# Kernel tuning notes

Measured on AMD Instinct MI355X. Metric: run time of the kernel, lower is better.

The kernel has to match this reference:

```python
import jax, jax.numpy as jnp
import numpy as np

IMG_H, IMG_W = 900, 1600
NUM_CLASSES = 10
NUM_CAMS = 6

# pcdet boxes_to_corners_3d corner template (unit box, centered)
CORNER_TEMPLATE = jnp.array(
    [[1, 1, -1], [1, -1, -1], [-1, -1, -1], [-1, 1, -1],
     [1, 1, 1], [1, -1, 1], [-1, -1, 1], [-1, 1, 1]], dtype=jnp.float32) * 0.5


def boxes_to_corners_3d(boxes):
    # boxes: [N,7] = (x,y,z,dx,dy,dz,heading) -> [N,8,3]
    dims = boxes[:, 3:6]
    corners = dims[:, None, :] * CORNER_TEMPLATE  # [N,8,3]
    yaw = boxes[:, 6]
    c, s = jnp.cos(yaw), jnp.sin(yaw)
    z = jnp.zeros_like(c)
    o = jnp.ones_like(c)
    # rotate_points_along_z: points @ [[c,s,0],[-s,c,0],[0,0,1]]
    rot = jnp.stack([c, s, z, -s, c, z, z, z, o], axis=-1).reshape(-1, 3, 3)
    corners = jnp.einsum('nkj,njm->nkm', corners, rot)
    return corners + boxes[:, None, 0:3]


def box_iou(a, b):
    # a: [M,4], b: [K,4] xyxy -> [M,K]
    lt = jnp.maximum(a[:, None, :2], b[None, :, :2])
    rb = jnp.minimum(a[:, None, 2:], b[None, :, 2:])
    wh = jnp.clip(rb - lt, 0.0)
    inter = wh[..., 0] * wh[..., 1]
    area_a = (a[:, 2] - a[:, 0]) * (a[:, 3] - a[:, 1])
    area_b = (b[:, 2] - b[:, 0]) * (b[:, 3] - b[:, 1])
    union = area_a[:, None] + area_b[None, :] - inter
    return jnp.where(union > 0, inter / union, 0.0)


def _project_boxes(pred_boxes, img_aug_matrix, lidar_aug_matrix, lidar2image):
    # batch index 0 (B=1); returns proj [6,N,4] and valid [6,N]
    N = pred_boxes.shape[0]
    corners = boxes_to_corners_3d(pred_boxes).reshape(-1, 3)  # [N*8,3]
    la = lidar_aug_matrix[0]
    pts = corners - la[:3, 3]
    pts = jnp.linalg.inv(la[:3, :3]) @ pts.T  # [3, N*8]
    l2i = lidar2image[0]
    cc = l2i[:, :3, :3] @ pts + l2i[:, :3, 3][:, :, None]  # [6,3,N*8]
    zc = jnp.clip(cc[:, 2, :], 1e-5, 1e5)
    xy = cc[:, :2, :] / zc[:, None, :]
    cc = jnp.concatenate([xy, zc[:, None, :]], axis=1)
    ia = img_aug_matrix[0]
    cc = ia[:, :3, :3] @ cc + ia[:, :3, 3][:, :, None]
    pix = jnp.transpose(cc[:, :2, :], (0, 2, 1))  # [6, N*8, 2]
    # .long() truncation (non-differentiable in original)
    pix = jax.lax.stop_gradient(pix).astype(jnp.int32)
    px = jnp.clip(pix[..., 0], 0, IMG_W)
    py = jnp.clip(pix[..., 1], 0, IMG_H)
    pix = jnp.stack([px, py], -1).reshape(NUM_CAMS, N, 8, 2).astype(pred_boxes.dtype)
    xy1 = pix.min(axis=2)  # [6,N,2]
    xy2 = pix.max(axis=2)
    valid = jnp.all((xy2 - xy1) > 0, axis=-1)  # [6,N]
    proj = jnp.concatenate([xy1, xy2], axis=-1)  # [6,N,4]
    return proj, valid


def setup_inputs() -> dict:
    rng = np.random.default_rng(0)
    N, M = 4096, 6144
    xy = rng.uniform(-40, 40, (N, 2))
    zc = rng.uniform(-1, 1, (N, 1))
    dims = rng.uniform(1.0, 4.0, (N, 3))
    yaw = rng.uniform(0, 2 * np.pi, (N, 1))
    pred_boxes = np.concatenate([xy, zc, dims, yaw], axis=1).astype(np.float32)
    # 6 cameras: pinhole intrinsics + yaw-spaced extrinsics
    K = np.array([[1000., 0., 800.], [0., 1000., 450.], [0., 0., 1.]])
    l2i = np.zeros((1, NUM_CAMS, 4, 4), np.float32)
    for ci, ang in enumerate(np.linspace(0, 2 * np.pi, NUM_CAMS, endpoint=False)):
        fwd = np.array([np.cos(ang), np.sin(ang), 0.])
        right = np.array([np.sin(ang), -np.cos(ang), 0.])
        down = np.array([0., 0., -1.])
        R = np.stack([right, down, fwd], 0)
        l2i[0, ci, :3, :3] = K @ R
        l2i[0, ci, 3, 3] = 1.0
    img_aug_matrix = np.tile(np.eye(4, dtype=np.float32), (1, NUM_CAMS, 1, 1))
    lidar_aug_matrix = np.eye(4, dtype=np.float32)[None]
    cx = rng.uniform(0, IMG_W, M)
    cy = rng.uniform(0, IMG_H, M)
    w = rng.uniform(20, 300, M)
    h = rng.uniform(20, 300, M)
    det_boxes = np.stack([np.clip(cx - w / 2, 0, IMG_W), np.clip(cy - h / 2, 0, IMG_H),
                          np.clip(cx + w / 2, 0, IMG_W), np.clip(cy + h / 2, 0, IMG_H)], 1).astype(np.float32)
    det_labels = rng.integers(1, NUM_CLASSES + 1, M).astype(np.int32)
    det_scores = rng.uniform(0.05, 1.0, M).astype(np.float32)
    det_batch_idx = np.zeros(M, np.int32)
    det_cam_idx = (np.arange(M) % NUM_CAMS).astype(np.int32)
    return {
        'pred_boxes': jnp.asarray(pred_boxes),
        'img_aug_matrix': jnp.asarray(img_aug_matrix),
        'lidar_aug_matrix': jnp.asarray(lidar_aug_matrix),
        'lidar2image': jnp.asarray(l2i),
        'det_boxes': jnp.asarray(det_boxes),
        'det_labels': jnp.asarray(det_labels),
        'det_scores': jnp.asarray(det_scores),
        'det_batch_idx': jnp.asarray(det_batch_idx),
        'det_cam_idx': jnp.asarray(det_cam_idx),
    }


def reference(pred_boxes, img_aug_matrix, lidar_aug_matrix, lidar2image,
              det_boxes, det_labels, det_scores, det_batch_idx, det_cam_idx):
    proj, valid = _project_boxes(pred_boxes, img_aug_matrix, lidar_aug_matrix, lidar2image)
    label_matrix = jax.nn.one_hot(det_labels - 1, NUM_CLASSES, dtype=det_scores.dtype) * det_scores[:, None]
    probs_sum = jnp.zeros((pred_boxes.shape[0], NUM_CLASSES), dtype=det_scores.dtype)
    for c in range(NUM_CAMS):
        mask = ((det_cam_idx == c) & (det_batch_idx == 0)).astype(det_boxes.dtype)
        iou = box_iou(det_boxes, proj[c]) * mask[:, None]  # [M,N]
        probs_sum = probs_sum + (iou.T @ label_matrix) * valid[c][:, None]  # [N,10]
    denom = 1e-5 + valid.astype(probs_sum.dtype).sum(axis=0)
    box_probs_mean = probs_sum / denom[:, None]
    pred_scores = jnp.nan_to_num(jnp.max(box_probs_mean, axis=-1), nan=0.0)
    pred_labels = jnp.argmax(box_probs_mean, axis=-1) + 1
    return pred_labels, pred_scores
```

## Files before the change

### kernel.cpp

```cpp
#include <hip/hip_runtime.h>
#include <cstdint>
#include <climits>

#pragma clang fp contract(off)

#define NCAM 6
#define NCLS 10
#define NKEY 60
#define IMGW 1600
#define IMGH 900
#define TBOX 4
#define CHUNK 512

__device__ __forceinline__ int sat_f2i(float f) {
    if (f != f) return 0;
    if (f >= 2147483648.0f) return INT_MAX;
    if (f <= -2147483648.0f) return INT_MIN;
    return (int)f;
}

__global__ __launch_bounds__(256) void prep_kernel(
        const float*  __restrict__ boxes,
        const float*  __restrict__ ia,
        const float*  __restrict__ la,
        const float*  __restrict__ l2i,
        const float4* __restrict__ det_boxes,
        const int*    __restrict__ det_labels,
        const float*  __restrict__ det_scores,
        const int*    __restrict__ det_batch,
        const int*    __restrict__ det_cam,
        float* __restrict__ projW,
        float* __restrict__ slab,
        int*   __restrict__ cnt,
        int N, int M, int PB, int CAPW) {
    int tid = threadIdx.x;

    if ((int)blockIdx.x < PB) {
        int n = blockIdx.x * 256 + tid;
        if (n >= N) return;
        float bx = boxes[n*7+0], by = boxes[n*7+1], bz = boxes[n*7+2];
        float dx = boxes[n*7+3], dy = boxes[n*7+4], dz = boxes[n*7+5];
        float yaw = boxes[n*7+6];
        float c = (float)cos((double)yaw);
        float s = (float)sin((double)yaw);

        float a00=la[0],a01=la[1],a02=la[2],t0=la[3];
        float a10=la[4],a11=la[5],a12=la[6],t1=la[7];
        float a20=la[8],a21=la[9],a22=la[10],t2=la[11];
        float det = a00*(a11*a22-a12*a21) - a01*(a10*a22-a12*a20) + a02*(a10*a21-a11*a20);
        float id = 1.0f/det;
        float r00=(a11*a22-a12*a21)*id, r01=(a02*a21-a01*a22)*id, r02=(a01*a12-a02*a11)*id;
        float r10=(a12*a20-a10*a22)*id, r11=(a00*a22-a02*a20)*id, r12=(a02*a10-a00*a12)*id;
        float r20=(a10*a21-a11*a20)*id, r21=(a01*a20-a00*a21)*id, r22=(a00*a11-a01*a10)*id;

        float PX[8], PY[8], PZ[8];
        #pragma unroll
        for (int k = 0; k < 8; k++) {
            float sx = ((k==0||k==1||k==4||k==5) ?  0.5f : -0.5f) * dx;
            float sy = ((k==0||k==3||k==4||k==7) ?  0.5f : -0.5f) * dy;
            float sz = ((k>=4)                   ?  0.5f : -0.5f) * dz;
            float cx = sx*c - sy*s + bx;
            float cy = sx*s + sy*c + by;
            float cz = sz + bz;
            float ux = cx - t0, uy = cy - t1, uz = cz - t2;
            PX[k] = r00*ux + r01*uy + r02*uz;
            PY[k] = r10*ux + r11*uy + r12*uz;
            PZ[k] = r20*ux + r21*uy + r22*uz;
        }
        for (int cam = 0; cam < NCAM; cam++) {
            const float* L = l2i + cam*16;
            const float* A = ia  + cam*16;
            int minx = INT_MAX, miny = INT_MAX, maxx = INT_MIN, maxy = INT_MIN;
            #pragma unroll
            for (int k = 0; k < 8; k++) {
                float u = L[0]*PX[k] + L[1]*PY[k] + L[2]*PZ[k]  + L[3];
                float v = L[4]*PX[k] + L[5]*PY[k] + L[6]*PZ[k]  + L[7];
                float w = L[8]*PX[k] + L[9]*PY[k] + L[10]*PZ[k] + L[11];
                float zc = fminf(fmaxf(w, 1e-5f), 100000.0f);
                float x = u / zc, y = v / zc;
                float xx = A[0]*x + A[1]*y + A[2]*zc + A[3];
                float yy = A[4]*x + A[5]*y + A[6]*zc + A[7];
                int pxi = sat_f2i(xx); pxi = min(max(pxi, 0), IMGW);
                int pyi = sat_f2i(yy); pyi = min(max(pyi, 0), IMGH);
                minx = min(minx, pxi); maxx = max(maxx, pxi);
                miny = min(miny, pyi); maxy = max(maxy, pyi);
            }
            float x1 = (float)minx, y1 = (float)miny, x2 = (float)maxx, y2 = (float)maxy;
            float validf = ((x2 - x1) > 0.0f && (y2 - y1) > 0.0f) ? 1.0f : 0.0f;
            projW[(cam*6+0)*N + n] = x1;
            projW[(cam*6+1)*N + n] = y1;
            projW[(cam*6+2)*N + n] = x2;
            projW[(cam*6+3)*N + n] = y2;
            projW[(cam*6+4)*N + n] = (x2 - x1) * (y2 - y1);
            projW[(cam*6+5)*N + n] = validf;
        }
        return;
    }

    int k = (int)blockIdx.x - PB;
    int cam = k / NCLS, cls = k % NCLS;
    int w = tid >> 6, lane = tid & 63;
    int per = (M + 3) >> 2;
    int m0 = w * per, m1 = min(m0 + per, M);
    float* base = slab + (size_t)(k * 4 + w) * CAPW * 8;
    int pos = 0;
    for (int c = m0; c < m1; c += 64) {
        int m = c + lane;
        bool pred = false;
        if (m < m1) {
            int dc = det_cam[m], db = det_batch[m], dl = det_labels[m] - 1;
            pred = (db == 0) && (dc == cam) && (dl == cls);
        }
        unsigned long long ball = __ballot(pred);
        if (pred) {
            int p = pos + __popcll(ball & ((1ull << lane) - 1ull));
            float4 b = det_boxes[m];
            float area = (b.z - b.x) * (b.w - b.y);
            float4* o = (float4*)(base + (size_t)p * 8);
            o[0] = b;
            o[1] = make_float4(area, det_scores[m], 0.0f, 0.0f);
        }
        pos += __popcll(ball);
    }
    if (lane == 0) cnt[k * 4 + w] = pos;
}

__global__ __launch_bounds__(256) void main_kernel(
        const float* __restrict__ projW,
        const float* __restrict__ slab,
        const int*   __restrict__ cnt,
        float*       __restrict__ partial,
        int N, int CAPW) {
    #pragma clang fp contract(fast)
    int tid = threadIdx.x;
    int k = blockIdx.y;
    int cam = k / NCLS;
    int box0 = blockIdx.x * (256 * TBOX) + tid;

    __shared__ float4 sbox[CHUNK];
    __shared__ float2 sq[CHUNK];

    float Px1[TBOX], Py1[TBOX], Px2[TBOX], Py2[TBOX], Pa[TBOX], Pv[TBOX], acc[TBOX];
    #pragma unroll
    for (int t = 0; t < TBOX; t++) {
        int b = box0 + t * 256;
        int bi = min(b, N - 1);
        Px1[t] = projW[(cam*6+0)*N + bi];
        Py1[t] = projW[(cam*6+1)*N + bi];
        Px2[t] = projW[(cam*6+2)*N + bi];
        Py2[t] = projW[(cam*6+3)*N + bi];
        Pa[t]  = projW[(cam*6+4)*N + bi];
        Pv[t]  = projW[(cam*6+5)*N + bi];
        acc[t] = 0.0f;
    }

    #pragma unroll
    for (int sub = 0; sub < 4; sub++) {
        int nk = cnt[k * 4 + sub];
        const float4* gb = (const float4*)(slab + (size_t)(k * 4 + sub) * CAPW * 8);
        for (int base = 0; base < nk; base += CHUNK) {
            int cc = min(CHUNK, nk - base);
            __syncthreads();
            for (int i = tid; i < cc; i += 256) {
                float4 b0 = gb[(size_t)(base + i) * 2];
                float4 b1 = gb[(size_t)(base + i) * 2 + 1];
                sbox[i] = b0;
                sq[i] = make_float2(b1.x, b1.y);
            }
            __syncthreads();
            for (int m = 0; m < cc; m++) {
                float4 b = sbox[m];
                float2 q = sq[m];
                #pragma unroll
                for (int t = 0; t < TBOX; t++) {
                    float ltx = fmaxf(b.x, Px1[t]);
                    float lty = fmaxf(b.y, Py1[t]);
                    float rbx = fminf(b.z, Px2[t]);
                    float rby = fminf(b.w, Py2[t]);
                    float iw = fmaxf(rbx - ltx, 0.0f);
                    float ih = fmaxf(rby - lty, 0.0f);
                    float inter = iw * ih;
                    float uni = (q.x + Pa[t]) - inter;
                    float r = __fdividef(inter, uni);
                    float iou = (uni > 0.0f) ? r : 0.0f;
                    acc[t] += iou * q.y;
                }
            }
        }
    }

    #pragma unroll
    for (int t = 0; t < TBOX; t++) {
        int b = box0 + t * 256;
        if (b < N) partial[(size_t)k * N + b] = acc[t] * Pv[t];
    }
}

__global__ __launch_bounds__(256) void reduce_kernel(
        const float* __restrict__ partial,
        const float* __restrict__ projW,
        float* __restrict__ out, int N) {
    int n = blockIdx.x * 256 + threadIdx.x;
    if (n >= N) return;
    float p[NCLS];
    #pragma unroll
    for (int c = 0; c < NCLS; c++) p[c] = 0.0f;
    #pragma unroll
    for (int cam = 0; cam < NCAM; cam++)
        #pragma unroll
        for (int c = 0; c < NCLS; c++)
            p[c] += partial[(size_t)(cam * NCLS + c) * N + n];
    float nv = 0.0f;
    #pragma unroll
    for (int cam = 0; cam < NCAM; cam++) nv += projW[(cam*6+5)*N + n];
    float denom = 1e-5f + nv;
    float best = -1e30f; int bk = 0;
    #pragma unroll
    for (int c = 0; c < NCLS; c++) {
        float v = p[c] / denom;
        if (v > best) { best = v; bk = c; }
    }
    out[n]     = (float)(bk + 1);
    out[N + n] = best;
}

extern "C" void kernel_launch(void* const* d_in, const int* in_sizes, int n_in,
                              void* d_out, int out_size, void* d_ws, size_t ws_size,
                              hipStream_t stream) {
    const float*  pred_boxes = (const float*)d_in[0];
    const float*  ia         = (const float*)d_in[1];
    const float*  la         = (const float*)d_in[2];
    const float*  l2i        = (const float*)d_in[3];
    const float4* det_boxes  = (const float4*)d_in[4];
    const int*    det_labels = (const int*)d_in[5];
    const float*  det_scores = (const float*)d_in[6];
    const int*    det_batch  = (const int*)d_in[7];
    const int*    det_cam    = (const int*)d_in[8];
    float* out = (float*)d_out;

    int N = in_sizes[0] / 7;
    int M = in_sizes[4] / 4;
    int PB = (N + 255) / 256;
    int BX = (N + 256*TBOX - 1) / (256*TBOX);
    int CAPW = (M + 3) / 4;

    char* w = (char*)d_ws;
    float* slab    = (float*)w;
    size_t off = (size_t)NKEY * 4 * CAPW * 8 * 4;
    float* projW   = (float*)(w + off);
    off += (size_t)36 * N * 4;
    float* partial = (float*)(w + off);
    off += (size_t)NKEY * N * 4;
    int*   cnt     = (int*)(w + off);

    prep_kernel<<<PB + NKEY, 256, 0, stream>>>(pred_boxes, ia, la, l2i,
                                               det_boxes, det_labels, det_scores,
                                               det_batch, det_cam,
                                               projW, slab, cnt, N, M, PB, CAPW);
    main_kernel<<<dim3(BX, NKEY), 256, 0, stream>>>(projW, slab, cnt, partial, N, CAPW);
    reduce_kernel<<<PB, 256, 0, stream>>>(partial, projW, out, N);
}
```

Before: 119.9 us.

## Split detection sub-slabs across grid z and fuse reduction via atomics and ticket

```diff
diff --git a/kernel.cpp b/kernel.cpp
--- a/kernel.cpp
+++ b/kernel.cpp
@@ -10,7 +10,8 @@
 #define IMGW 1600
 #define IMGH 900
 #define TBOX 4
-#define CHUNK 512
+#define CHUNK 256
+#define ZB 4
 
 __device__ __forceinline__ int sat_f2i(float f) {
     if (f != f) return 0;
@@ -32,11 +33,22 @@
         float* __restrict__ projW,
         float* __restrict__ slab,
         int*   __restrict__ cnt,
-        int N, int M, int PB, int CAPW) {
+        float* __restrict__ probs,
+        int*   __restrict__ ticket,
+        int N, int M, int PB, int CAPW, int BX) {
     int tid = threadIdx.x;
-
-    if ((int)blockIdx.x < PB) {
-        int n = blockIdx.x * 256 + tid;
+    int bid = (int)blockIdx.x;
+
+    if (bid >= PB + NKEY) {
+        int zb = bid - (PB + NKEY);
+        int ZT = NCLS * N;
+        for (int i = zb * 256 + tid; i < ZT; i += ZB * 256) probs[i] = 0.0f;
+        if (zb == 0 && tid < BX) ticket[tid] = 0;
+        return;
+    }
+
+    if (bid < PB) {
+        int n = bid * 256 + tid;
         if (n >= N) return;
         float bx = boxes[n*7+0], by = boxes[n*7+1], bz = boxes[n*7+2];
         float dx = boxes[n*7+3], dy = boxes[n*7+4], dz = boxes[n*7+5];
@@ -97,7 +109,7 @@
         return;
     }
 
-    int k = (int)blockIdx.x - PB;
+    int k = bid - PB;
     int cam = k / NCLS, cls = k % NCLS;
     int w = tid >> 6, lane = tid & 63;
     int per = (M + 3) >> 2;
@@ -129,16 +141,21 @@
         const float* __restrict__ projW,
         const float* __restrict__ slab,
         const int*   __restrict__ cnt,
-        float*       __restrict__ partial,
+        float*       __restrict__ probs,
+        int*         __restrict__ ticket,
+        float*       __restrict__ out,
         int N, int CAPW) {
     #pragma clang fp contract(fast)
     int tid = threadIdx.x;
     int k = blockIdx.y;
-    int cam = k / NCLS;
-    int box0 = blockIdx.x * (256 * TBOX) + tid;
+    int z = blockIdx.z;
+    int cam = k / NCLS, cls = k % NCLS;
+    int bx = blockIdx.x;
+    int box0 = bx * (256 * TBOX) + tid;
 
     __shared__ float4 sbox[CHUNK];
     __shared__ float2 sq[CHUNK];
+    __shared__ int is_last;
 
     float Px1[TBOX], Py1[TBOX], Px2[TBOX], Py2[TBOX], Pa[TBOX], Pv[TBOX], acc[TBOX];
     #pragma unroll
@@ -154,37 +171,34 @@
         acc[t] = 0.0f;
     }
 
-    #pragma unroll
-    for (int sub = 0; sub < 4; sub++) {
-        int nk = cnt[k * 4 + sub];
-        const float4* gb = (const float4*)(slab + (size_t)(k * 4 + sub) * CAPW * 8);
-        for (int base = 0; base < nk; base += CHUNK) {
-            int cc = min(CHUNK, nk - base);
-            __syncthreads();
-            for (int i = tid; i < cc; i += 256) {
-                float4 b0 = gb[(size_t)(base + i) * 2];
-                float4 b1 = gb[(size_t)(base + i) * 2 + 1];
-                sbox[i] = b0;
-                sq[i] = make_float2(b1.x, b1.y);
-            }
-            __syncthreads();
-            for (int m = 0; m < cc; m++) {
-                float4 b = sbox[m];
-                float2 q = sq[m];
-                #pragma unroll
-                for (int t = 0; t < TBOX; t++) {
-                    float ltx = fmaxf(b.x, Px1[t]);
-                    float lty = fmaxf(b.y, Py1[t]);
-                    float rbx = fminf(b.z, Px2[t]);
-                    float rby = fminf(b.w, Py2[t]);
-                    float iw = fmaxf(rbx - ltx, 0.0f);
-                    float ih = fmaxf(rby - lty, 0.0f);
-                    float inter = iw * ih;
-                    float uni = (q.x + Pa[t]) - inter;
-                    float r = __fdividef(inter, uni);
-                    float iou = (uni > 0.0f) ? r : 0.0f;
-                    acc[t] += iou * q.y;
-                }
+    int nk = cnt[k * 4 + z];
+    const float4* gb = (const float4*)(slab + (size_t)(k * 4 + z) * CAPW * 8);
+    for (int base = 0; base < nk; base += CHUNK) {
+        int cc = min(CHUNK, nk - base);
+        __syncthreads();
+        for (int i = tid; i < cc; i += 256) {
+            float4 b0 = gb[(size_t)(base + i) * 2];
+            float4 b1 = gb[(size_t)(base + i) * 2 + 1];
+            sbox[i] = b0;
+            sq[i] = make_float2(b1.x, b1.y);
+        }
+        __syncthreads();
+        for (int m = 0; m < cc; m++) {
+            float4 b = sbox[m];
+            float2 q = sq[m];
+            #pragma unroll
+            for (int t = 0; t < TBOX; t++) {
+                float ltx = fmaxf(b.x, Px1[t]);
+                float lty = fmaxf(b.y, Py1[t]);
+                float rbx = fminf(b.z, Px2[t]);
+                float rby = fminf(b.w, Py2[t]);
+                float iw = fmaxf(rbx - ltx, 0.0f);
+                float ih = fmaxf(rby - lty, 0.0f);
+                float inter = iw * ih;
+                float uni = (q.x + Pa[t]) - inter;
+                float r = __fdividef(inter, uni);
+                float iou = (uni > 0.0f) ? r : 0.0f;
+                acc[t] += iou * q.y;
             }
         }
     }
@@ -192,36 +206,39 @@
     #pragma unroll
     for (int t = 0; t < TBOX; t++) {
         int b = box0 + t * 256;
-        if (b < N) partial[(size_t)k * N + b] = acc[t] * Pv[t];
-    }
-}
-
-__global__ __launch_bounds__(256) void reduce_kernel(
-        const float* __restrict__ partial,
-        const float* __restrict__ projW,
-        float* __restrict__ out, int N) {
-    int n = blockIdx.x * 256 + threadIdx.x;
-    if (n >= N) return;
-    float p[NCLS];
+        float v = acc[t] * Pv[t];
+        if (b < N && v != 0.0f) atomicAdd(&probs[(size_t)cls * N + b], v);
+    }
+
+    __syncthreads();
+    if (tid == 0) {
+        __threadfence();
+        int old = atomicAdd(&ticket[bx], 1);
+        is_last = (old == NKEY * 4 - 1) ? 1 : 0;
+    }
+    __syncthreads();
+    if (!is_last) return;
+    __threadfence();
+
     #pragma unroll
-    for (int c = 0; c < NCLS; c++) p[c] = 0.0f;
-    #pragma unroll
-    for (int cam = 0; cam < NCAM; cam++)
+    for (int t = 0; t < TBOX; t++) {
+        int b = box0 + t * 256;
+        if (b >= N) continue;
+        float nv = 0.0f;
         #pragma unroll
-        for (int c = 0; c < NCLS; c++)
-            p[c] += partial[(size_t)(cam * NCLS + c) * N + n];
-    float nv = 0.0f;
-    #pragma unroll
-    for (int cam = 0; cam < NCAM; cam++) nv += projW[(cam*6+5)*N + n];
-    float denom = 1e-5f + nv;
-    float best = -1e30f; int bk = 0;
-    #pragma unroll
-    for (int c = 0; c < NCLS; c++) {
-        float v = p[c] / denom;
-        if (v > best) { best = v; bk = c; }
-    }
-    out[n]     = (float)(bk + 1);
-    out[N + n] = best;
+        for (int c2 = 0; c2 < NCAM; c2++) nv += projW[(c2*6+5)*N + b];
+        float denom = 1e-5f + nv;
+        float best = -1e30f; int bk = 0;
+        #pragma unroll
+        for (int c2 = 0; c2 < NCLS; c2++) {
+            float p = __hip_atomic_load(&probs[(size_t)c2 * N + b],
+                                        __ATOMIC_RELAXED, __HIP_MEMORY_SCOPE_AGENT);
+            float v = p / denom;
+            if (v > best) { best = v; bk = c2; }
+        }
+        out[b]     = (float)(bk + 1);
+        out[N + b] = best;
+    }
 }
 
 extern "C" void kernel_launch(void* const* d_in, const int* in_sizes, int n_in,
@@ -245,18 +262,19 @@
     int CAPW = (M + 3) / 4;
 
     char* w = (char*)d_ws;
-    float* slab    = (float*)w;
+    float* slab   = (float*)w;
     size_t off = (size_t)NKEY * 4 * CAPW * 8 * 4;
-    float* projW   = (float*)(w + off);
+    float* projW  = (float*)(w + off);
     off += (size_t)36 * N * 4;
-    float* partial = (float*)(w + off);
-    off += (size_t)NKEY * N * 4;
-    int*   cnt     = (int*)(w + off);
-
-    prep_kernel<<<PB + NKEY, 256, 0, stream>>>(pred_boxes, ia, la, l2i,
-                                               det_boxes, det_labels, det_scores,
-                                               det_batch, det_cam,
-                                               projW, slab, cnt, N, M, PB, CAPW);
-    main_kernel<<<dim3(BX, NKEY), 256, 0, stream>>>(projW, slab, cnt, partial, N, CAPW);
-    reduce_kernel<<<PB, 256, 0, stream>>>(partial, projW, out, N);
-}
+    float* probs  = (float*)(w + off);
+    off += (size_t)NCLS * N * 4;
+    int*   cnt    = (int*)(w + off);
+    off += 256 * 4;
+    int*   ticket = (int*)(w + off);
+
+    prep_kernel<<<PB + NKEY + ZB, 256, 0, stream>>>(
+        pred_boxes, ia, la, l2i, det_boxes, det_labels, det_scores,
+        det_batch, det_cam, projW, slab, cnt, probs, ticket, N, M, PB, CAPW, BX);
+    main_kernel<<<dim3(BX, NKEY, 4), 256, 0, stream>>>(
+        projW, slab, cnt, probs, ticket, out, N, CAPW);
+}
```

Measured after the change: 119.7 us. Within noise of the previous version (-0.2%).
